# Optimization experiments

Measured on AMD Instinct MI355X. Metric: run time of the kernel, lower is better.

The kernel has to match this reference:

```python
import jax, jax.numpy as jnp
import numpy as np

B, S, D, H = 2, 2048, 1024, 16
DK = D // H
LARGE = 1e9
LN_EPS = 1e-5


def sinusoidal_embeddings(seq_len, d):
    pos = jnp.arange(seq_len, dtype=jnp.float32)[:, None]          # [S,1]
    i = jnp.arange(d // 2, dtype=jnp.float32)[None, :]             # [1,d/2]
    freq = jnp.exp(-(2.0 * i / d) * jnp.log(10000.0))
    ang = pos * freq                                               # [S,d/2]
    pe = jnp.zeros((seq_len, d), dtype=jnp.float32)
    pe = pe.at[:, 0::2].set(jnp.sin(ang))
    pe = pe.at[:, 1::2].set(jnp.cos(ang))
    return pe


def setup_inputs() -> dict:
    key = jax.random.key(0)
    ks = jax.random.split(key, 6)
    sc = 1.0 / np.sqrt(D)
    return {
        "X": jax.random.normal(ks[0], (B, S, D), jnp.float32),
        "W_q": jax.random.normal(ks[1], (D, D), jnp.float32) * sc,
        "W_k": jax.random.normal(ks[2], (D, D), jnp.float32) * sc,
        "W_v": jax.random.normal(ks[3], (D, D), jnp.float32) * sc,
        "W_o": jax.random.normal(ks[4], (D, D), jnp.float32) * sc,
        "alpha": jnp.ones((1, H, S - 1, 1), jnp.float32),
        "ln_scale": jnp.ones((D,), jnp.float32),
        "ln_bias": jnp.zeros((D,), jnp.float32),
    }


def reference(X, W_q, W_k, W_v, W_o, alpha, ln_scale, ln_bias):
    # projections (torch Linear: x @ W.T), split heads -> [B,H,S,dk]
    def proj(W):
        return jnp.einsum('bsd,ed->bse', X, W).reshape(B, S, H, DK).transpose(0, 2, 1, 3)
    Q, K, V = proj(W_q), proj(W_k), proj(W_v)

    # EMA smear on K along sequence
    a = jax.nn.sigmoid(alpha)                                      # [1,H,S-1,1]
    smeared = K[:, :, 1:, :] * a + K[:, :, :-1, :] * (1.0 - a)
    K = jnp.concatenate([K[:, :, 0:1, :], smeared], axis=2)

    # inline sinusoidal positional embeddings added to K and Q
    pe = sinusoidal_embeddings(S, DK)                              # [S,dk]
    K = K + pe
    Q = Q + pe

    mask = jnp.triu(jnp.ones((S, S), jnp.float32), k=1) * (-LARGE)
    scores = jnp.einsum('bhqd,bhkd->bhqk', Q, K) / jnp.sqrt(jnp.float32(DK)) + mask
    weights = jax.nn.softmax(scores, axis=-1)
    attn = jnp.einsum('bhqk,bhkd->bhqd', weights, V)               # [B,H,S,dk]
    attn = attn.transpose(0, 2, 1, 3).reshape(B, S, D)

    Y = jnp.einsum('bsd,ed->bse', attn, W_o) + X

    # LayerNorm
    mu = jnp.mean(Y, axis=-1, keepdims=True)
    var = jnp.mean(jnp.square(Y - mu), axis=-1, keepdims=True)
    Y = (Y - mu) / jnp.sqrt(var + LN_EPS) * ln_scale + ln_bias
    return Y
```

## Files before the change

### kernel.cpp

```cpp
#include <hip/hip_runtime.h>


#define LB __launch_bounds__(256)

typedef unsigned short u16;
typedef unsigned int u32;
typedef __attribute__((ext_vector_type(2))) unsigned int u32x2;
typedef __attribute__((ext_vector_type(4))) unsigned short us4;
typedef __attribute__((ext_vector_type(8))) unsigned short us8;
typedef __attribute__((ext_vector_type(8))) __bf16 bf8;
typedef __attribute__((ext_vector_type(4))) float f4;
typedef __attribute__((ext_vector_type(4))) short s4;

#define QSCALE 0.18033688011112042f

#if __has_builtin(__builtin_amdgcn_exp2f)
#define EXP2 __builtin_amdgcn_exp2f
#else
#define EXP2 exp2f
#endif

static __device__ __forceinline__ float bf2f(u16 h) {
  union { unsigned int u; float f; } c; c.u = ((unsigned int)h) << 16; return c.f;
}
static __device__ __forceinline__ u16 f2bf(float f) {
  union { float f; unsigned int u; } c; c.f = f;
  unsigned int u = c.u + 0x7FFFu + ((c.u >> 16) & 1u);
  return (u16)(u >> 16);
}
#if __has_builtin(__builtin_amdgcn_cvt_pk_bf16_f32)
typedef __attribute__((ext_vector_type(2))) __bf16 bf2v;
static __device__ __forceinline__ us4 pk_bf16x4(f4 v) {
  bf2v lo = __builtin_amdgcn_cvt_pk_bf16_f32(v[0], v[1]);
  bf2v hi = __builtin_amdgcn_cvt_pk_bf16_f32(v[2], v[3]);
  u32x2 r = {__builtin_bit_cast(u32, lo), __builtin_bit_cast(u32, hi)};
  return __builtin_bit_cast(us4, r);
}
#else
static __device__ __forceinline__ us4 pk_bf16x4(f4 v) {
  return us4{f2bf(v[0]), f2bf(v[1]), f2bf(v[2]), f2bf(v[3])};
}
#endif
static __device__ __forceinline__ float pe_val(int s, int dk) {
  float fr = __expf((float)(dk & ~1) * (-9.210340371976184f / 64.0f));
  float ang = (float)s * fr;
  return (dk & 1) ? __cosf(ang) : __sinf(ang);
}

#if __has_builtin(__builtin_amdgcn_mfma_f32_16x16x16bf16_1k)
static __device__ __forceinline__ f4 mfma16(us4 a, us4 b, f4 c) {
  return __builtin_amdgcn_mfma_f32_16x16x16bf16_1k(
      __builtin_bit_cast(s4, a), __builtin_bit_cast(s4, b), c, 0, 0, 0);
}
#elif __has_builtin(__builtin_amdgcn_mfma_f32_16x16x16_bf16)
typedef __attribute__((ext_vector_type(4))) __bf16 bf4;
static __device__ __forceinline__ f4 mfma16(us4 a, us4 b, f4 c) {
  return __builtin_amdgcn_mfma_f32_16x16x16_bf16(
      __builtin_bit_cast(bf4, a), __builtin_bit_cast(bf4, b), c, 0, 0, 0);
}
#else
static __device__ __forceinline__ f4 mfma16(us4 a, us4 b, f4 c) {
  asm volatile("v_mfma_f32_16x16x16_bf16 %0, %1, %2, %0" : "+v"(c) : "v"(a), "v"(b));
  return c;
}
#endif

#define GLDS(gp, lp) __builtin_amdgcn_global_load_lds( \
    (const __attribute__((address_space(1))) void*)(gp), \
    (__attribute__((address_space(3))) void*)(lp), 16, 0, 0)

__global__ LB void cvt_kernel(const float* __restrict__ X, const float* __restrict__ Wq,
                              const float* __restrict__ Wk, const float* __restrict__ Wv,
                              const float* __restrict__ Wo, u16* __restrict__ Xb,
                              u16* __restrict__ Wcat, u16* __restrict__ Wob) {
  const unsigned t = blockIdx.x * 256 + threadIdx.x;
  const float* src; u16* dst; size_t off;
  if (t < (512u << 10))      { src = X;  dst = Xb;                off = t; }
  else if (t < (640u << 10)) { src = Wq; dst = Wcat;              off = t - (512u << 10); }
  else if (t < (768u << 10)) { src = Wk; dst = Wcat + (1u << 20); off = t - (640u << 10); }
  else if (t < (896u << 10)) { src = Wv; dst = Wcat + (2u << 20); off = t - (768u << 10); }
  else                       { src = Wo; dst = Wob;               off = t - (896u << 10); }
  off *= 8;
  f4 a = *(const f4*)(src + off);
  f4 b = *(const f4*)(src + off + 4);
  us8 o = {f2bf(a[0]), f2bf(a[1]), f2bf(a[2]), f2bf(a[3]),
           f2bf(b[0]), f2bf(b[1]), f2bf(b[2]), f2bf(b[3])};
  *(us8*)(dst + off) = o;
}

static __device__ __forceinline__ void gemm_core(
    const u16* __restrict__ Abase, const u16* __restrict__ Bbase,
    u16* Als, u16* Bls, int m0, int n0, int tid, f4 acc[4][4]) {
  const int w = tid >> 6, lane = tid & 63;
  const int l16 = lane & 15, quad = lane >> 4;
  const int wm = w & 1, wn = w >> 1;
  for (int kk = 0; kk < 1024; kk += 32) {
    __syncthreads();
#pragma unroll
    for (int it = 0; it < 2; it++) {
      int cb = (w * 2 + it) * 64;
      int c = cb + lane;
      int row = c >> 2, kc = c & 3;
      GLDS(Abase + (size_t)(m0 + row) * 1024 + kk + kc * 8, &Als[cb * 8]);
      GLDS(Bbase + (size_t)(n0 + row) * 1024 + kk + kc * 8, &Bls[cb * 8]);
    }
    __syncthreads();
    bf8 af[4], bfr[4];
#pragma unroll
    for (int mt = 0; mt < 4; mt++)
      af[mt] = __builtin_bit_cast(bf8, *(const us8*)(&Als[(wm * 64 + mt * 16 + l16) * 32 + quad * 8]));
#pragma unroll
    for (int nt = 0; nt < 4; nt++)
      bfr[nt] = __builtin_bit_cast(bf8, *(const us8*)(&Bls[(wn * 64 + nt * 16 + l16) * 32 + quad * 8]));
#pragma unroll
    for (int mt = 0; mt < 4; mt++)
#pragma unroll
      for (int nt = 0; nt < 4; nt++)
        acc[mt][nt] = __builtin_amdgcn_mfma_f32_16x16x32_bf16(af[mt], bfr[nt], acc[mt][nt], 0, 0, 0);
  }
}

__global__ LB void gemm_qkv(const u16* __restrict__ Xb, const u16* __restrict__ Wcat,
                            u16* __restrict__ Qb, u16* __restrict__ Kraw,
                            u16* __restrict__ Vp) {
  __shared__ u16 Als[128 * 32];
  __shared__ u16 Bls[128 * 32];
  const int tid = threadIdx.x;
  const int m0 = blockIdx.y * 128, n0 = blockIdx.x * 128;
  f4 acc[4][4];
#pragma unroll
  for (int a = 0; a < 4; a++)
#pragma unroll
    for (int b = 0; b < 4; b++) acc[a][b] = f4{0.f, 0.f, 0.f, 0.f};
  gemm_core(Xb, Wcat, Als, Bls, m0, n0, tid, acc);

  const int w = tid >> 6, lane = tid & 63;
  const int l16 = lane & 15, quad = lane >> 4;
  const int wm = w & 1, wn = w >> 1;
  const int z = blockIdx.x >> 3;
#pragma unroll
  for (int mt = 0; mt < 4; mt++)
#pragma unroll
    for (int nt = 0; nt < 4; nt++)
#pragma unroll
      for (int r = 0; r < 4; r++) {
        int m = m0 + wm * 64 + mt * 16 + quad * 4 + r;
        int nn = (n0 + wn * 64 + nt * 16 + l16) & 1023;
        float v = acc[mt][nt][r];
        int b = m >> 11, s = m & 2047, h = nn >> 6, dk = nn & 63;
        size_t bhoff = (size_t)(b * 16 + h) * (2048 * 64);
        if (z == 0) {
          Qb[bhoff + (size_t)s * 64 + dk] = f2bf((v + pe_val(s, dk)) * QSCALE);
        } else if (z == 1) {
          Kraw[bhoff + (size_t)s * 64 + dk] = f2bf(v);
        } else {
          int kb = s >> 6, sl = s & 63;
          int t = sl >> 4, Qq = (sl >> 2) & 3, jj = sl & 3;
          int dn = dk >> 4, lv = dk & 15;
          Vp[bhoff + (size_t)kb * 4096 + ((t * 4 + dn) * 64 + Qq * 16 + lv) * 4 + jj] = f2bf(v);
        }
      }
}

__global__ LB void ema_pe(const u16* __restrict__ Kraw, const float* __restrict__ alpha,
                          u16* __restrict__ Kp) {
  int idx = blockIdx.x * 256 + threadIdx.x;
  int b8  = idx & 7;
  int s   = (idx >> 3) & 2047;
  int bh  = idx >> 14;
  int dk8 = b8 * 8;
  size_t base = ((size_t)bh * 2048 + s) * 64 + dk8;
  us8 kc = *(const us8*)(Kraw + base);
  float kv[8];
#pragma unroll
  for (int j = 0; j < 8; j++) kv[j] = bf2f(kc[j]);
  if (s > 0) {
    us8 kp = *(const us8*)(Kraw + base - 64);
    float aa = alpha[(bh & 15) * 2047 + s - 1];
    float a = 1.0f / (1.0f + __expf(-aa));
#pragma unroll
    for (int j = 0; j < 8; j++) kv[j] = kv[j] * a + bf2f(kp[j]) * (1.0f - a);
  }
  us8 o;
#pragma unroll
  for (int j = 0; j < 8; j++) o[j] = f2bf(kv[j] + pe_val(s, dk8 + j));
  int kt16 = s >> 4, c = b8 >> 2, quad = b8 & 3, l16s = s & 15;
  size_t off = (size_t)bh * (2048 * 64) + (size_t)kt16 * 1024 + (c * 64 + quad * 16 + l16s) * 8;
  *(us8*)(Kp + off) = o;
}

template<bool MASK>
static __device__ __forceinline__ void attn_step_lds(
    const u16* kbase, const u16* vbase,
    const bf8* qf, f4* acc, float& lsum, int lane, int quad, int qrel0) {
  f4 sc[4];
#pragma unroll
  for (int t = 0; t < 4; t++) sc[t] = f4{0.f, 0.f, 0.f, 0.f};
#pragma unroll
  for (int t = 0; t < 4; t++)
#pragma unroll
    for (int c = 0; c < 2; c++) {
      bf8 kf = __builtin_bit_cast(bf8, *(const us8*)(kbase + (t * 2 + c) * 512 + lane * 8));
      sc[t] = __builtin_amdgcn_mfma_f32_16x16x32_bf16(kf, qf[c], sc[t], 0, 0, 0);
    }
  us4 pf[4];
#pragma unroll
  for (int t = 0; t < 4; t++) {
    f4 pv;
#pragma unroll
    for (int r = 0; r < 4; r++) {
      float s = sc[t][r];
      if (MASK && (t * 16 + quad * 4 + r > qrel0)) s = -1e30f;
      float p = EXP2(s);
      lsum += p;
      pv[r] = p;
    }
    pf[t] = pk_bf16x4(pv);
  }
#pragma unroll
  for (int t = 0; t < 4; t++)
#pragma unroll
    for (int dn = 0; dn < 4; dn++) {
      us4 vf = *(const us4*)(vbase + ((t * 4 + dn) * 64 + lane) * 4);
      acc[dn] = mfma16(vf, pf[t], acc[dn]);
    }
}

__global__ LB void attn_kernel(const u16* __restrict__ Qb, const u16* __restrict__ Kp,
                               const u16* __restrict__ Vp, u16* __restrict__ Ab) {
  __shared__ u16 Kls[2][4096];
  __shared__ u16 Vls[2][4096];
  const int tid = threadIdx.x, w = tid >> 6, lane = tid & 63;
  const int l16 = lane & 15, quad = lane >> 4;
  const int idx = blockIdx.x;
  const int bh = idx & 31;
  const int p  = idx >> 5;
  const size_t bhoff = (size_t)bh * (2048 * 64);
  const u16* Kt = Kp + bhoff;
  const u16* Vt = Vp + bhoff;
  const int b = bh >> 4, h = bh & 15;

  for (int ph = 0; ph < 2; ph++) {
    const int g = ph ? p : 31 - p;
    const int T = g + 1;
    const int qw = g * 64 + w * 16;

    bf8 qf[2];
#pragma unroll
    for (int c = 0; c < 2; c++)
      qf[c] = __builtin_bit_cast(bf8, *(const us8*)(Qb + bhoff + (size_t)(qw + l16) * 64 + c * 32 + quad * 8));

    f4 acc[4];
#pragma unroll
    for (int dn = 0; dn < 4; dn++) acc[dn] = f4{0.f, 0.f, 0.f, 0.f};
    float lsum = 0.f;

    {
      const u16* kg = Kt + w * 1024;
      const u16* vg = Vt + w * 1024;
      GLDS(kg + lane * 8,       &Kls[0][w * 1024]);
      GLDS(kg + 512 + lane * 8, &Kls[0][w * 1024 + 512]);
      GLDS(vg + lane * 8,       &Vls[0][w * 1024]);
      GLDS(vg + 512 + lane * 8, &Vls[0][w * 1024 + 512]);
    }
    asm volatile("s_waitcnt vmcnt(0)" ::: "memory");
    __builtin_amdgcn_s_barrier();

    for (int kb = 0; kb < T; kb++) {
      const int cur = kb & 1;
      if (kb + 1 < T) {
        const u16* kg = Kt + (size_t)(kb + 1) * 4096 + w * 1024;
        const u16* vg = Vt + (size_t)(kb + 1) * 4096 + w * 1024;
        u16* kl = &Kls[cur ^ 1][w * 1024];
        u16* vl = &Vls[cur ^ 1][w * 1024];
        GLDS(kg + lane * 8, kl);
        GLDS(kg + 512 + lane * 8, kl + 512);
        GLDS(vg + lane * 8, vl);
        GLDS(vg + 512 + lane * 8, vl + 512);
      }
      if (kb == T - 1)
        attn_step_lds<true>(&Kls[cur][0], &Vls[cur][0], qf, acc, lsum, lane, quad, w * 16 + l16);
      else
        attn_step_lds<false>(&Kls[cur][0], &Vls[cur][0], qf, acc, lsum, lane, quad, 0);
      asm volatile("s_waitcnt vmcnt(0)" ::: "memory");
      __builtin_amdgcn_s_barrier();
    }

    lsum += __shfl_xor(lsum, 16, 64);
    lsum += __shfl_xor(lsum, 32, 64);
    float rinv = 1.0f / lsum;
    const int q = qw + l16;
    u16* orow = Ab + ((size_t)(b * 2048 + q)) * 1024 + h * 64;
#pragma unroll
    for (int dn = 0; dn < 4; dn++) {
      us4 o = pk_bf16x4(f4{acc[dn][0] * rinv, acc[dn][1] * rinv,
                           acc[dn][2] * rinv, acc[dn][3] * rinv});
      *(us4*)(orow + dn * 16 + quad * 4) = o;
    }
  }
}

__global__ LB void gemm_out(const u16* __restrict__ Ab, const u16* __restrict__ Wob,
                            const float* __restrict__ X, float* __restrict__ Yp) {
  __shared__ u16 Als[64 * 32];
  __shared__ u16 Bls[128 * 32];
  const int tid = threadIdx.x;
  const int m0 = blockIdx.y * 64, n0 = blockIdx.x * 128;
  const int w = tid >> 6, lane = tid & 63;
  const int l16 = lane & 15, quad = lane >> 4;
  f4 acc[4][2];
#pragma unroll
  for (int a = 0; a < 4; a++)
#pragma unroll
    for (int b = 0; b < 2; b++) acc[a][b] = f4{0.f, 0.f, 0.f, 0.f};

  for (int kk = 0; kk < 1024; kk += 32) {
    __syncthreads();
    {
      int cb = w * 64;
      int c = cb + lane;
      int row = c >> 2, kc = c & 3;
      GLDS(Ab + (size_t)(m0 + row) * 1024 + kk + kc * 8, &Als[cb * 8]);
    }
#pragma unroll
    for (int it = 0; it < 2; it++) {
      int cb = (w * 2 + it) * 64;
      int c = cb + lane;
      int row = c >> 2, kc = c & 3;
      GLDS(Wob + (size_t)(n0 + row) * 1024 + kk + kc * 8, &Bls[cb * 8]);
    }
    __syncthreads();
    bf8 af[4], bfr[2];
#pragma unroll
    for (int mt = 0; mt < 4; mt++)
      af[mt] = __builtin_bit_cast(bf8, *(const us8*)(&Als[(mt * 16 + l16) * 32 + quad * 8]));
#pragma unroll
    for (int nt = 0; nt < 2; nt++)
      bfr[nt] = __builtin_bit_cast(bf8, *(const us8*)(&Bls[(w * 32 + nt * 16 + l16) * 32 + quad * 8]));
#pragma unroll
    for (int mt = 0; mt < 4; mt++)
#pragma unroll
      for (int nt = 0; nt < 2; nt++)
        acc[mt][nt] = __builtin_amdgcn_mfma_f32_16x16x32_bf16(af[mt], bfr[nt], acc[mt][nt], 0, 0, 0);
  }

#pragma unroll
  for (int mt = 0; mt < 4; mt++)
#pragma unroll
    for (int nt = 0; nt < 2; nt++)
#pragma unroll
      for (int r = 0; r < 4; r++) {
        int m = m0 + mt * 16 + quad * 4 + r;
        int n = n0 + w * 32 + nt * 16 + l16;
        size_t o = (size_t)m * 1024 + n;
        Yp[o] = acc[mt][nt][r] + X[o];
      }
}

__global__ LB void ln_kernel(const float* __restrict__ Y, const float* __restrict__ g,
                             const float* __restrict__ bta, float* __restrict__ out) {
  __shared__ float ls[4], lsq[4];
  const int row = blockIdx.x, tid = threadIdx.x;
  const int w = tid >> 6, lane = tid & 63;
  f4 v = *(const f4*)(Y + (size_t)row * 1024 + tid * 4);
  float s  = v[0] + v[1] + v[2] + v[3];
  float sq = v[0] * v[0] + v[1] * v[1] + v[2] * v[2] + v[3] * v[3];
#pragma unroll
  for (int d = 1; d < 64; d <<= 1) { s += __shfl_xor(s, d, 64); sq += __shfl_xor(sq, d, 64); }
  if (lane == 0) { ls[w] = s; lsq[w] = sq; }
  __syncthreads();
  s  = ls[0] + ls[1] + ls[2] + ls[3];
  sq = lsq[0] + lsq[1] + lsq[2] + lsq[3];
  float mu  = s * (1.0f / 1024.0f);
  float var = sq * (1.0f / 1024.0f) - mu * mu;
  float rs  = rsqrtf(var + 1e-5f);
  f4 o;
#pragma unroll
  for (int j = 0; j < 4; j++) {
    int col = tid * 4 + j;
    o[j] = (v[j] - mu) * rs * g[col] + bta[col];
  }
  *(f4*)(out + (size_t)row * 1024 + tid * 4) = o;
}

extern "C" void kernel_launch(void* const* d_in, const int* in_sizes, int n_in,
                              void* d_out, int out_size, void* d_ws, size_t ws_size,
                              hipStream_t stream) {
  (void)in_sizes; (void)n_in; (void)out_size; (void)ws_size;
  const float* X  = (const float*)d_in[0];
  const float* Wq = (const float*)d_in[1];
  const float* Wk = (const float*)d_in[2];
  const float* Wv = (const float*)d_in[3];
  const float* Wo = (const float*)d_in[4];
  const float* al = (const float*)d_in[5];
  const float* g  = (const float*)d_in[6];
  const float* bt = (const float*)d_in[7];

  char* ws = (char*)d_ws;
  float* Yp   = (float*)(ws);
  u16*   Xb   = (u16*)(ws + ((size_t)16 << 20));
  u16*   Wcat = (u16*)(ws + ((size_t)24 << 20));
  u16*   Wob  = (u16*)(ws + ((size_t)30 << 20));
  u16*   Qb   = (u16*)(ws + ((size_t)32 << 20));
  u16*   Kraw = (u16*)(ws + ((size_t)40 << 20));
  u16*   Ab   = (u16*)(ws + ((size_t)40 << 20));
  u16*   Kp   = (u16*)(ws + ((size_t)48 << 20));
  u16*   Vp   = (u16*)(ws + ((size_t)56 << 20));

  cvt_kernel<<<dim3(4096), 256, 0, stream>>>(X, Wq, Wk, Wv, Wo, Xb, Wcat, Wob);
  gemm_qkv<<<dim3(24, 32), 256, 0, stream>>>(Xb, Wcat, Qb, Kraw, Vp);
  ema_pe<<<dim3(2048), 256, 0, stream>>>(Kraw, al, Kp);
  attn_kernel<<<dim3(512), 256, 0, stream>>>(Qb, Kp, Vp, Ab);
  gemm_out<<<dim3(8, 64), 256, 0, stream>>>(Ab, Wob, X, Yp);
  ln_kernel<<<dim3(4096), 256, 0, stream>>>(Yp, g, bt, (float*)d_out);
}
```

Baseline: 192.3 us.

## Rewrite QKV GEMM as 256x256 tile with double-buffered swizzled LDS pipeline

Replaces the 128x128, K=32 single-buffered QKV projection GEMM with a 256x256 tile per 512-thread block. It uses K=64 double-buffered LDS halves, XOR-swizzled to avoid bank conflicts, and staggers async global-to-LDS loads across four quadrant phases with s_setprio around the MFMA bursts. The goal is to hide global load latency and raise arithmetic intensity. The costs are much more LDS (128KB) and register pressure, and only 192 blocks, which may underfill the 256 CUs.

```diff
diff --git a/kernel.cpp b/kernel.cpp
--- a/kernel.cpp
+++ b/kernel.cpp
@@ -68,6 +68,14 @@
 #define GLDS(gp, lp) __builtin_amdgcn_global_load_lds( \
     (const __attribute__((address_space(1))) void*)(gp), \
     (__attribute__((address_space(3))) void*)(lp), 16, 0, 0)
+
+#if __has_builtin(__builtin_amdgcn_s_setprio)
+#define SETPRIO(n) __builtin_amdgcn_s_setprio(n)
+#else
+#define SETPRIO(n) asm volatile("s_setprio " #n)
+#endif
+#define SB       asm volatile("s_barrier" ::: "memory")
+#define DRAIN(n) asm volatile("s_waitcnt vmcnt(" #n ")" ::: "memory")
 
 __global__ LB void cvt_kernel(const float* __restrict__ X, const float* __restrict__ Wq,
                               const float* __restrict__ Wk, const float* __restrict__ Wv,
@@ -88,64 +96,106 @@
   *(us8*)(dst + off) = o;
 }
 
-static __device__ __forceinline__ void gemm_core(
-    const u16* __restrict__ Abase, const u16* __restrict__ Bbase,
-    u16* Als, u16* Bls, int m0, int n0, int tid, f4 acc[4][4]) {
+static __device__ __forceinline__ void stageH(const u16* __restrict__ G, int grow0, int gcol0,
+                                              u16* lds, int tid) {
+#pragma unroll
+  for (int hh = 0; hh < 2; hh++) {
+    int c = tid + hh * 512;
+    int row = c >> 3, cb = (c & 7) * 16;
+    int cbs = cb ^ ((row & 7) << 4);
+    GLDS(G + (size_t)(grow0 + row) * 1024 + gcol0 + (cbs >> 1), lds + (size_t)c * 8);
+  }
+}
+static __device__ __forceinline__ bf8 ldsfrag(const u16* base, int row, int k2, int quad) {
+  int cb = (k2 * 64 + quad * 16) ^ ((row & 7) << 4);
+  return __builtin_bit_cast(bf8, *(const us8*)(base + row * 64 + (cb >> 1)));
+}
+
+#define QPHASE(MH, NH, AH, BH, STAGE, VM) do {                                   \
+  bf8 af_[4][2], bv_[2][2];                                                      \
+  _Pragma("unroll") for (int q_ = 0; q_ < 4; q_++) {                             \
+    int row_ = q_ * 32 + wm * 16 + l16;                                          \
+    _Pragma("unroll") for (int k2_ = 0; k2_ < 2; k2_++)                          \
+      af_[q_][k2_] = ldsfrag((AH), row_, k2_, quad);                             \
+  }                                                                              \
+  _Pragma("unroll") for (int j_ = 0; j_ < 2; j_++) {                             \
+    int row_ = j_ * 64 + wn * 16 + l16;                                          \
+    _Pragma("unroll") for (int k2_ = 0; k2_ < 2; k2_++)                          \
+      bv_[j_][k2_] = ldsfrag((BH), row_, k2_, quad);                             \
+  }                                                                              \
+  STAGE;                                                                         \
+  VM;                                                                            \
+  SB;                                                                            \
+  SETPRIO(1);                                                                    \
+  _Pragma("unroll") for (int q_ = 0; q_ < 4; q_++)                               \
+    _Pragma("unroll") for (int j_ = 0; j_ < 2; j_++)                             \
+      _Pragma("unroll") for (int k2_ = 0; k2_ < 2; k2_++)                        \
+        acc[(MH) * 4 + q_][(NH) * 2 + j_] = __builtin_amdgcn_mfma_f32_16x16x32_bf16( \
+            af_[q_][k2_], bv_[j_][k2_], acc[(MH) * 4 + q_][(NH) * 2 + j_], 0, 0, 0); \
+  SETPRIO(0);                                                                    \
+  SB;                                                                            \
+} while (0)
+
+__global__ __launch_bounds__(512, 2) void gemm_qkv(
+    const u16* __restrict__ Xb, const u16* __restrict__ Wcat,
+    u16* __restrict__ Qb, u16* __restrict__ Kraw, u16* __restrict__ Vp) {
+  __shared__ u16 LA[2][2][128 * 64];
+  __shared__ u16 LBs[2][2][128 * 64];
+  const int tid = threadIdx.x;
   const int w = tid >> 6, lane = tid & 63;
   const int l16 = lane & 15, quad = lane >> 4;
   const int wm = w & 1, wn = w >> 1;
-  for (int kk = 0; kk < 1024; kk += 32) {
-    __syncthreads();
-#pragma unroll
-    for (int it = 0; it < 2; it++) {
-      int cb = (w * 2 + it) * 64;
-      int c = cb + lane;
-      int row = c >> 2, kc = c & 3;
-      GLDS(Abase + (size_t)(m0 + row) * 1024 + kk + kc * 8, &Als[cb * 8]);
-      GLDS(Bbase + (size_t)(n0 + row) * 1024 + kk + kc * 8, &Bls[cb * 8]);
-    }
-    __syncthreads();
-    bf8 af[4], bfr[4];
-#pragma unroll
-    for (int mt = 0; mt < 4; mt++)
-      af[mt] = __builtin_bit_cast(bf8, *(const us8*)(&Als[(wm * 64 + mt * 16 + l16) * 32 + quad * 8]));
+  const int m0 = blockIdx.y * 256, n0 = blockIdx.x * 256;
+
+  f4 acc[8][4];
+#pragma unroll
+  for (int a = 0; a < 8; a++)
+#pragma unroll
+    for (int b = 0; b < 4; b++) acc[a][b] = f4{0.f, 0.f, 0.f, 0.f};
+
+  stageH(Xb,   m0,       0, &LA[0][0][0], tid);
+  stageH(Wcat, n0,       0, &LBs[0][0][0], tid);
+  stageH(Xb,   m0 + 128, 0, &LA[0][1][0], tid);
+  stageH(Wcat, n0 + 128, 0, &LBs[0][1][0], tid);
+  stageH(Xb,   m0,      64, &LA[1][0][0], tid);
+  stageH(Wcat, n0,      64, &LBs[1][0][0], tid);
+  DRAIN(4);
+  SB;
+
+  for (int i = 0; i < 8; i++) {
+    const int k1  = (2 * i + 1) * 64;
+    const int k2c = (2 * i + 2) * 64;
+    const int k3  = (2 * i + 3) * 64;
+    const bool s2 = (2 * i + 2) < 16, s3 = (2 * i + 3) < 16;
+    QPHASE(0, 0, &LA[0][0][0], &LBs[0][0][0],
+           stageH(Xb, m0 + 128, k1, &LA[1][1][0], tid), (void)0);
+    QPHASE(0, 1, &LA[0][0][0], &LBs[0][1][0],
+           stageH(Wcat, n0 + 128, k1, &LBs[1][1][0], tid), (void)0);
+    QPHASE(1, 0, &LA[0][1][0], &LBs[0][0][0],
+           { if (s2) stageH(Xb, m0, k2c, &LA[0][0][0], tid); }, (void)0);
+    QPHASE(1, 1, &LA[0][1][0], &LBs[0][1][0],
+           { if (s2) stageH(Wcat, n0, k2c, &LBs[0][0][0], tid); },
+           { if (i == 7) { DRAIN(0); } else { DRAIN(4); } });
+    QPHASE(0, 0, &LA[1][0][0], &LBs[1][0][0],
+           { if (s2) stageH(Xb, m0 + 128, k2c, &LA[0][1][0], tid); }, (void)0);
+    QPHASE(0, 1, &LA[1][0][0], &LBs[1][1][0],
+           { if (s2) stageH(Wcat, n0 + 128, k2c, &LBs[0][1][0], tid); }, (void)0);
+    QPHASE(1, 0, &LA[1][1][0], &LBs[1][0][0],
+           { if (s3) stageH(Xb, m0, k3, &LA[1][0][0], tid); }, (void)0);
+    QPHASE(1, 1, &LA[1][1][0], &LBs[1][1][0],
+           { if (s3) stageH(Wcat, n0, k3, &LBs[1][0][0], tid); },
+           DRAIN(4));
+  }
+
+  const int z = blockIdx.x >> 2;
+#pragma unroll
+  for (int mt = 0; mt < 8; mt++)
 #pragma unroll
     for (int nt = 0; nt < 4; nt++)
-      bfr[nt] = __builtin_bit_cast(bf8, *(const us8*)(&Bls[(wn * 64 + nt * 16 + l16) * 32 + quad * 8]));
-#pragma unroll
-    for (int mt = 0; mt < 4; mt++)
-#pragma unroll
-      for (int nt = 0; nt < 4; nt++)
-        acc[mt][nt] = __builtin_amdgcn_mfma_f32_16x16x32_bf16(af[mt], bfr[nt], acc[mt][nt], 0, 0, 0);
-  }
-}
-
-__global__ LB void gemm_qkv(const u16* __restrict__ Xb, const u16* __restrict__ Wcat,
-                            u16* __restrict__ Qb, u16* __restrict__ Kraw,
-                            u16* __restrict__ Vp) {
-  __shared__ u16 Als[128 * 32];
-  __shared__ u16 Bls[128 * 32];
-  const int tid = threadIdx.x;
-  const int m0 = blockIdx.y * 128, n0 = blockIdx.x * 128;
-  f4 acc[4][4];
-#pragma unroll
-  for (int a = 0; a < 4; a++)
-#pragma unroll
-    for (int b = 0; b < 4; b++) acc[a][b] = f4{0.f, 0.f, 0.f, 0.f};
-  gemm_core(Xb, Wcat, Als, Bls, m0, n0, tid, acc);
-
-  const int w = tid >> 6, lane = tid & 63;
-  const int l16 = lane & 15, quad = lane >> 4;
-  const int wm = w & 1, wn = w >> 1;
-  const int z = blockIdx.x >> 3;
-#pragma unroll
-  for (int mt = 0; mt < 4; mt++)
-#pragma unroll
-    for (int nt = 0; nt < 4; nt++)
 #pragma unroll
       for (int r = 0; r < 4; r++) {
-        int m = m0 + wm * 64 + mt * 16 + quad * 4 + r;
-        int nn = (n0 + wn * 64 + nt * 16 + l16) & 1023;
+        int m = m0 + mt * 32 + wm * 16 + quad * 4 + r;
+        int nn = (n0 + nt * 64 + wn * 16 + l16) & 1023;
         float v = acc[mt][nt][r];
         int b = m >> 11, s = m & 2047, h = nn >> 6, dk = nn & 63;
         size_t bhoff = (size_t)(b * 16 + h) * (2048 * 64);
@@ -408,7 +458,7 @@
   u16*   Vp   = (u16*)(ws + ((size_t)56 << 20));
 
   cvt_kernel<<<dim3(4096), 256, 0, stream>>>(X, Wq, Wk, Wv, Wo, Xb, Wcat, Wob);
-  gemm_qkv<<<dim3(24, 32), 256, 0, stream>>>(Xb, Wcat, Qb, Kraw, Vp);
+  gemm_qkv<<<dim3(12, 16), 512, 0, stream>>>(Xb, Wcat, Qb, Kraw, Vp);
   ema_pe<<<dim3(2048), 256, 0, stream>>>(Kraw, al, Kp);
   attn_kernel<<<dim3(512), 256, 0, stream>>>(Qb, Kp, Vp, Ab);
   gemm_out<<<dim3(8, 64), 256, 0, stream>>>(Ab, Wob, X, Yp);
```

Result: slower. 199.4 us (+3.7%).
